# Kernel optimization log

Hardware: AMD Instinct MI355X
Metric: run time of the kernel (lower is better)

The kernel has to match this reference:

```python
import jax, jax.numpy as jnp
import numpy as np

HIDDEN = 256
HEADS = 8
HEAD_DIM = HIDDEN // HEADS
SCALE = HEAD_DIM ** -0.5


def setup_inputs() -> dict:
    key = jax.random.key(0)
    ks = jax.random.split(key, 12)
    B, N = 2, 2048
    s = lambda fan_in: 1.0 / np.sqrt(fan_in)
    inp = {
        'x': jax.random.normal(ks[0], (B, N, HIDDEN), jnp.float32),
        'coords': jax.random.normal(ks[1], (B, N, 3), jnp.float32),
        'W_qkv': jax.random.normal(ks[2], (HIDDEN, 3 * HIDDEN), jnp.float32) * s(HIDDEN),
        'W_out': jax.random.normal(ks[3], (HIDDEN, HIDDEN), jnp.float32) * s(HIDDEN),
        'b_out': jnp.zeros((HIDDEN,), jnp.float32),
        'pos_w1': jax.random.normal(ks[4], (3, 16), jnp.float32) * s(3),
        'pos_b1': jnp.zeros((16,), jnp.float32),
        'pos_w2': jax.random.normal(ks[5], (16, HEADS), jnp.float32) * s(16),
        'pos_b2': jnp.zeros((HEADS,), jnp.float32),
        'sym_w1': jax.random.normal(ks[6], (3, 16), jnp.float32) * s(3),
        'sym_b1': jnp.zeros((16,), jnp.float32),
        'sym_w2': jax.random.normal(ks[7], (16, HEADS), jnp.float32) * s(16),
        'sym_b2': jnp.zeros((HEADS,), jnp.float32),
    }
    return inp


def _bias_mlp(rel, w1, b1, w2, b2):
    # rel: [B,N,N,3] -> [B,H,N,N]
    h = jax.nn.relu(jnp.einsum('bijc,ck->bijk', rel, w1) + b1)
    out = jnp.einsum('bijk,kh->bijh', h, w2) + b2
    return jnp.transpose(out, (0, 3, 1, 2))


def reference(x, coords, W_qkv, W_out, b_out, pos_w1, pos_b1, pos_w2, pos_b2,
              sym_w1, sym_b1, sym_w2, sym_b2):
    B, N, C = x.shape
    qkv = (x @ W_qkv).reshape(B, N, 3, HEADS, HEAD_DIM)
    qkv = jnp.transpose(qkv, (2, 0, 3, 1, 4))  # [3,B,H,N,D]
    q, k, v = qkv[0], qkv[1], qkv[2]
    dots = jnp.einsum('bhid,bhjd->bhij', q, k) * SCALE
    rel_pos = coords[:, :, None, :] - coords[:, None, :, :]  # [B,N,N,3]
    reflect = jnp.array([-1.0, 1.0, 1.0], dtype=coords.dtype)
    coords_sym = coords * reflect
    sym_rel_pos = coords[:, :, None, :] - coords_sym[:, None, :, :]
    bias_direct = _bias_mlp(rel_pos, pos_w1, pos_b1, pos_w2, pos_b2)
    bias_sym = _bias_mlp(sym_rel_pos, sym_w1, sym_b1, sym_w2, sym_b2)
    attn = jax.nn.softmax(dots + bias_direct + bias_sym, axis=-1)
    out = jnp.einsum('bhij,bhjd->bhid', attn, v)
    out = jnp.transpose(out, (0, 2, 1, 3)).reshape(B, N, C)
    return out @ W_out + b_out
```

## Files before the change

kernel.cpp:

```cpp
#include <hip/hip_runtime.h>
#include <hip/hip_fp16.h>

typedef _Float16 half8_t __attribute__((ext_vector_type(8)));
typedef _Float16 half4_t __attribute__((ext_vector_type(4)));
typedef _Float16 h2      __attribute__((ext_vector_type(2)));
typedef float    f32x4   __attribute__((ext_vector_type(4)));

#define LOG2E 1.4426950408889634f
#define KSCALE (0.17677669529663687f * LOG2E)

#if __has_builtin(__builtin_amdgcn_exp2f)
#define EXP2F(x) __builtin_amdgcn_exp2f(x)
#else
#define EXP2F(x) exp2f(x)
#endif

template <int N>
__device__ __forceinline__ int dpp_ror(int v) {
  return __builtin_amdgcn_update_dpp(0, v, 0x120 + N, 0xf, 0xf, true);
}
__device__ __forceinline__ h2 rowmax16_h2(h2 v) {
  int t;
  t = dpp_ror<1>(__builtin_bit_cast(int, v));
  v = __builtin_elementwise_max(v, __builtin_bit_cast(h2, t));
  t = dpp_ror<2>(__builtin_bit_cast(int, v));
  v = __builtin_elementwise_max(v, __builtin_bit_cast(h2, t));
  t = dpp_ror<4>(__builtin_bit_cast(int, v));
  v = __builtin_elementwise_max(v, __builtin_bit_cast(h2, t));
  t = dpp_ror<8>(__builtin_bit_cast(int, v));
  v = __builtin_elementwise_max(v, __builtin_bit_cast(h2, t));
  return v;
}

__global__ __launch_bounds__(256) void prep_misc(
    const float* __restrict__ x, const float* __restrict__ Wqkv,
    const float* __restrict__ Wout, const float* __restrict__ coords,
    const float* __restrict__ pw1, const float* __restrict__ pb1,
    const float* __restrict__ sw1, const float* __restrict__ sb1,
    _Float16* __restrict__ xf16, _Float16* __restrict__ WqkvT,
    _Float16* __restrict__ WoutT, _Float16* __restrict__ APre,
    _Float16* __restrict__ BPre)
{
  __shared__ float tile[64][65];
  const int bi = blockIdx.x, tid = threadIdx.x;
  if (bi < 1024) {
    const int idx = bi * 256 + tid;
    f32x4 v = *reinterpret_cast<const f32x4*>(x + idx * 4);
    half4_t h;
    h[0] = (_Float16)v[0]; h[1] = (_Float16)v[1];
    h[2] = (_Float16)v[2]; h[3] = (_Float16)v[3];
    *reinterpret_cast<half4_t*>(xf16 + idx * 4) = h;
  } else if (bi < 1088) {
    const float* src; _Float16* dst; int t, W;
    if (bi < 1072) { t = bi - 1024; src = Wqkv; dst = WqkvT; W = 768; }
    else           { t = bi - 1072; src = Wout; dst = WoutT; W = 256; }
    const int nOT = W >> 6;
    const int tk = t / nOT, to = t % nOT;
    const int cx = tid & 63, ry = tid >> 6;
#pragma unroll
    for (int rr = 0; rr < 16; ++rr) {
      const int kl = rr * 4 + ry;
      tile[kl][cx] = src[(tk * 64 + kl) * W + to * 64 + cx];
    }
    __syncthreads();
#pragma unroll
    for (int rr = 0; rr < 16; ++rr) {
      const int ol = rr * 4 + ry;
      dst[(to * 64 + ol) * 256 + tk * 64 + cx] = (_Float16)tile[cx][ol];
    }
  } else {
    const int row = (bi - 1088) * 256 + tid;
    const float c0 = coords[row * 3 + 0];
    const float c1 = coords[row * 3 + 1];
    const float c2 = coords[row * 3 + 2];
#pragma unroll
    for (int k = 0; k < 16; ++k) {
      float a = c0 * pw1[k] + c1 * pw1[16 + k] + c2 * pw1[32 + k];
      APre[row * 32 + k] = (_Float16)(a + pb1[k]);
      BPre[row * 32 + k] = (_Float16)a;
      float s  =  c0 * sw1[k] + c1 * sw1[16 + k] + c2 * sw1[32 + k];
      float sb = -c0 * sw1[k] + c1 * sw1[16 + k] + c2 * sw1[32 + k];
      APre[row * 32 + 16 + k] = (_Float16)(s + sb1[k]);
      BPre[row * 32 + 16 + k] = (_Float16)sb;
    }
  }
}

__global__ __launch_bounds__(256) void qkv_gemm(
    const _Float16* __restrict__ xf16, const _Float16* __restrict__ WqkvT,
    _Float16* __restrict__ Qh, _Float16* __restrict__ Kh,
    _Float16* __restrict__ Vt)
{
  __shared__ _Float16 vtile[4][64][24];
  const int wv = threadIdx.x >> 6;
  const int wg = blockIdx.x * 4 + wv;
  const int ti = wg / 12, og = wg % 12;
  const int i0 = ti * 16, o0 = og * 64;
  const int lane = threadIdx.x & 63, q = lane >> 4, c = lane & 15;
  f32x4 acc[4] = {{0,0,0,0},{0,0,0,0},{0,0,0,0},{0,0,0,0}};
  const _Float16* arow = xf16 + (i0 + c) * 256;
  const _Float16* brow = WqkvT + (o0 + c) * 256;
#pragma unroll
  for (int k0 = 0; k0 < 256; k0 += 32) {
    half8_t af = *reinterpret_cast<const half8_t*>(arow + k0 + q * 8);
#pragma unroll
    for (int t = 0; t < 4; ++t) {
      half8_t bf = *reinterpret_cast<const half8_t*>(brow + t * 16 * 256 + k0 + q * 8);
      acc[t] = __builtin_amdgcn_mfma_f32_16x16x32_f16(af, bf, acc[t], 0, 0, 0);
    }
  }
  const int b = i0 >> 11, n0 = i0 & 2047;
  if (og < 8) {
#pragma unroll
    for (int t = 0; t < 4; ++t) {
      const int o = o0 + t * 16 + c;
      const int which = o >> 8, h = (o >> 5) & 7, d = o & 31;
#pragma unroll
      for (int r = 0; r < 4; ++r) {
        const int n = n0 + q * 4 + r;
        _Float16 v = (_Float16)acc[t][r];
        if (which == 0) Qh[((b * 8 + h) * 2048 + n) * 32 + d] = v;
        else            Kh[((b * 8 + h) * 2048 + n) * 32 + d] = v;
      }
    }
  } else {
    _Float16* vt = &vtile[wv][0][0];
#pragma unroll
    for (int t = 0; t < 4; ++t)
#pragma unroll
      for (int r = 0; r < 4; ++r)
        vt[(t * 16 + c) * 24 + q * 4 + r] = (_Float16)acc[t][r];
    asm volatile("s_waitcnt lgkmcnt(0)" ::: "memory");
    __builtin_amdgcn_sched_barrier(0);
    const long row = (long)(b * 256 + (o0 - 512) + lane);
    half8_t r0 = *reinterpret_cast<const half8_t*>(vt + lane * 24);
    half8_t r1 = *reinterpret_cast<const half8_t*>(vt + lane * 24 + 8);
    *reinterpret_cast<half8_t*>(Vt + row * 2048 + n0)     = r0;
    *reinterpret_cast<half8_t*>(Vt + row * 2048 + n0 + 8) = r1;
  }
}

__global__ __launch_bounds__(512, 4) void flash(
    const _Float16* __restrict__ Qh, const _Float16* __restrict__ Kh,
    const _Float16* __restrict__ Vt, const _Float16* __restrict__ APre,
    const _Float16* __restrict__ BPre, const float* __restrict__ pw2,
    const float* __restrict__ sw2, _Float16* __restrict__ Opart,
    float* __restrict__ Mpart)
{
  __shared__ __align__(16) unsigned char smem[53504];
  _Float16* biasH = reinterpret_cast<_Float16*>(smem);
  _Float16* pbuf  = reinterpret_cast<_Float16*>(smem + 37120);

  const int blk = blockIdx.x;
  const int b     = blk >> 8;
  const int chunk = (blk >> 6) & 3;
  const int i0    = (blk & 63) << 5;
  const int tid = threadIdx.x;
  const int w = tid >> 6, lane = tid & 63;
  const int q = lane >> 4, c = lane & 15;

  const _Float16* qbase = Qh + ((b * 8 + w) * 2048 + i0) * 32;
  half8_t qfA = *reinterpret_cast<const half8_t*>(qbase + c * 32 + q * 8);
  half8_t qfB = *reinterpret_cast<const half8_t*>(qbase + (16 + c) * 32 + q * 8);
  const _Float16* abase = APre + (b * 2048 + i0) * 32;
  half8_t apfA = *reinterpret_cast<const half8_t*>(abase + c * 32 + q * 8);
  half8_t apfB = *reinterpret_cast<const half8_t*>(abase + (16 + c) * 32 + q * 8);

  half8_t w2f;
#pragma unroll
  for (int jj = 0; jj < 8; ++jj) {
    const int k = q * 8 + jj;
    float val = 0.f;
    if (c < 8) val = (k < 16 ? pw2[k * 8 + c] : sw2[(k - 16) * 8 + c]) * LOG2E;
    w2f[jj] = (_Float16)val;
  }
  half8_t ones8;
#pragma unroll
  for (int jj = 0; jj < 8; ++jj) ones8[jj] = (_Float16)1.0f;

  float mA[4], mB[4];
  f32x4 O0A = {0,0,0,0}, O1A = {0,0,0,0}, O0B = {0,0,0,0}, O1B = {0,0,0,0};
  f32x4 lpA = {0,0,0,0}, lpB = {0,0,0,0};
#pragma unroll
  for (int r = 0; r < 4; ++r) { mA[r] = 0.f; mB[r] = 0.f; }

  const f32x4 z4 = {0.f, 0.f, 0.f, 0.f};
  half8_t hzero8 = {};

  const int jbase = chunk * 512;
  const _Float16* BPre_b = BPre + (long)b * 2048 * 32;
  _Float16* pbA = pbuf + w * 1024;
  _Float16* pbB = pbA + 512;

  for (int jt = 0; jt < 16; ++jt) {
    const int j0 = jbase + jt * 32;
    _Float16* bW = biasH + (jt & 1) * 9280;

#pragma unroll
    for (int mt = 0; mt < 4; ++mt) {
      const int jl = w * 4 + mt;
      half8_t bpf = *reinterpret_cast<const half8_t*>(
          BPre_b + (j0 + jl) * 32 + q * 8);
      half8_t hvA = __builtin_elementwise_max(apfA - bpf, hzero8);
      f32x4 bcA = __builtin_amdgcn_mfma_f32_16x16x32_f16(hvA, w2f, z4, 0, 0, 0);
      half8_t hvB = __builtin_elementwise_max(apfB - bpf, hzero8);
      f32x4 bcB = __builtin_amdgcn_mfma_f32_16x16x32_f16(hvB, w2f, z4, 0, 0, 0);
      if (c < 8) {
        half4_t b4;
        b4[0] = (_Float16)bcA[0]; b4[1] = (_Float16)bcA[1];
        b4[2] = (_Float16)bcA[2]; b4[3] = (_Float16)bcA[3];
        *reinterpret_cast<half4_t*>(bW + c * 1160 + jl * 36 + q * 4) = b4;
        half4_t b5;
        b5[0] = (_Float16)bcB[0]; b5[1] = (_Float16)bcB[1];
        b5[2] = (_Float16)bcB[2]; b5[3] = (_Float16)bcB[3];
        *reinterpret_cast<half4_t*>(bW + c * 1160 + jl * 36 + 16 + q * 4) = b5;
      }
    }

    const _Float16* kbase = Kh + ((b * 8 + w) * 2048 + j0) * 32;
    half8_t kf0 = *reinterpret_cast<const half8_t*>(kbase + (2 * c) * 32 + q * 8);
    half8_t kf1 = *reinterpret_cast<const half8_t*>(kbase + (2 * c + 1) * 32 + q * 8);
    const _Float16* vbase = Vt + (b * 8 + w) * 65536 + j0;
    half8_t vf0 = *reinterpret_cast<const half8_t*>(vbase + c * 2048 + q * 8);
    half8_t vf1 = *reinterpret_cast<const half8_t*>(vbase + (16 + c) * 2048 + q * 8);
    f32x4 sA0 = __builtin_amdgcn_mfma_f32_16x16x32_f16(qfA, kf0, z4, 0, 0, 0);
    f32x4 sA1 = __builtin_amdgcn_mfma_f32_16x16x32_f16(qfA, kf1, z4, 0, 0, 0);
    f32x4 sB0 = __builtin_amdgcn_mfma_f32_16x16x32_f16(qfB, kf0, z4, 0, 0, 0);
    f32x4 sB1 = __builtin_amdgcn_mfma_f32_16x16x32_f16(qfB, kf1, z4, 0, 0, 0);

    __syncthreads();

    const _Float16* bR = biasH + (jt & 1) * 9280 + w * 1160;
    half4_t bbA0 = *reinterpret_cast<const half4_t*>(bR + (2 * c) * 36 + q * 4);
    half4_t bbA1 = *reinterpret_cast<const half4_t*>(bR + (2 * c + 1) * 36 + q * 4);
    half4_t bbB0 = *reinterpret_cast<const half4_t*>(bR + (2 * c) * 36 + 16 + q * 4);
    half4_t bbB1 = *reinterpret_cast<const half4_t*>(bR + (2 * c + 1) * 36 + 16 + q * 4);

    {
      float sv0[4], sv1[4], p0[4], p1[4], mr[4];
#pragma unroll
      for (int r = 0; r < 4; ++r) {
        sv0[r] = sA0[r] * KSCALE + (float)bbA0[r];
        sv1[r] = sA1[r] * KSCALE + (float)bbA1[r];
        mr[r] = fmaxf(sv0[r], sv1[r]);
      }
#pragma unroll
      for (int r = 0; r < 4; ++r) {
        p0[r] = EXP2F(sv0[r] - mA[r]);
        p1[r] = EXP2F(sv1[r] - mA[r]);
      }
      float need = fmaxf(fmaxf(mr[0] - mA[0], mr[1] - mA[1]),
                         fmaxf(mr[2] - mA[2], mr[3] - mA[3]));
      if (__any(need > 4.0f)) {
        h2 pk01, pk23;
        pk01[0] = (_Float16)mr[0]; pk01[1] = (_Float16)mr[1];
        pk23[0] = (_Float16)mr[2]; pk23[1] = (_Float16)mr[3];
        pk01 = rowmax16_h2(pk01);
        pk23 = rowmax16_h2(pk23);
        float mred[4] = {(float)pk01[0], (float)pk01[1],
                         (float)pk23[0], (float)pk23[1]};
#pragma unroll
        for (int r = 0; r < 4; ++r) {
          const float mnew = fmaxf(mA[r], mred[r]);
          const float alpha = EXP2F(mA[r] - mnew);
          p0[r] *= alpha; p1[r] *= alpha;
          lpA[r] *= alpha;
          O0A[r] *= alpha; O1A[r] *= alpha;
          mA[r] = mnew;
        }
      }
#pragma unroll
      for (int r = 0; r < 4; ++r) {
        h2 pp; pp[0] = (_Float16)p0[r]; pp[1] = (_Float16)p1[r];
        *reinterpret_cast<h2*>(pbA + (q * 4 + r) * 32 + 2 * c) = pp;
      }
    }
    {
      float sv0[4], sv1[4], p0[4], p1[4], mr[4];
#pragma unroll
      for (int r = 0; r < 4; ++r) {
        sv0[r] = sB0[r] * KSCALE + (float)bbB0[r];
        sv1[r] = sB1[r] * KSCALE + (float)bbB1[r];
        mr[r] = fmaxf(sv0[r], sv1[r]);
      }
#pragma unroll
      for (int r = 0; r < 4; ++r) {
        p0[r] = EXP2F(sv0[r] - mB[r]);
        p1[r] = EXP2F(sv1[r] - mB[r]);
      }
      float need = fmaxf(fmaxf(mr[0] - mB[0], mr[1] - mB[1]),
                         fmaxf(mr[2] - mB[2], mr[3] - mB[3]));
      if (__any(need > 4.0f)) {
        h2 pk01, pk23;
        pk01[0] = (_Float16)mr[0]; pk01[1] = (_Float16)mr[1];
        pk23[0] = (_Float16)mr[2]; pk23[1] = (_Float16)mr[3];
        pk01 = rowmax16_h2(pk01);
        pk23 = rowmax16_h2(pk23);
        float mred[4] = {(float)pk01[0], (float)pk01[1],
                         (float)pk23[0], (float)pk23[1]};
#pragma unroll
        for (int r = 0; r < 4; ++r) {
          const float mnew = fmaxf(mB[r], mred[r]);
          const float alpha = EXP2F(mB[r] - mnew);
          p0[r] *= alpha; p1[r] *= alpha;
          lpB[r] *= alpha;
          O0B[r] *= alpha; O1B[r] *= alpha;
          mB[r] = mnew;
        }
      }
#pragma unroll
      for (int r = 0; r < 4; ++r) {
        h2 pp; pp[0] = (_Float16)p0[r]; pp[1] = (_Float16)p1[r];
        *reinterpret_cast<h2*>(pbB + (q * 4 + r) * 32 + 2 * c) = pp;
      }
    }

    asm volatile("s_waitcnt lgkmcnt(0)" ::: "memory");
    __builtin_amdgcn_sched_barrier(0);

    half8_t pfA = *reinterpret_cast<const half8_t*>(pbA + c * 32 + q * 8);
    half8_t pfB = *reinterpret_cast<const half8_t*>(pbB + c * 32 + q * 8);
    O0A = __builtin_amdgcn_mfma_f32_16x16x32_f16(pfA, vf0, O0A, 0, 0, 0);
    O1A = __builtin_amdgcn_mfma_f32_16x16x32_f16(pfA, vf1, O1A, 0, 0, 0);
    O0B = __builtin_amdgcn_mfma_f32_16x16x32_f16(pfB, vf0, O0B, 0, 0, 0);
    O1B = __builtin_amdgcn_mfma_f32_16x16x32_f16(pfB, vf1, O1B, 0, 0, 0);
    lpA = __builtin_amdgcn_mfma_f32_16x16x32_f16(pfA, ones8, lpA, 0, 0, 0);
    lpB = __builtin_amdgcn_mfma_f32_16x16x32_f16(pfB, ones8, lpB, 0, 0, 0);
  }

#pragma unroll
  for (int r = 0; r < 4; ++r) {
    const float s = lpA[r];
    const float inv = 1.f / s;
    const int n = i0 + q * 4 + r;
    const long base = (long)(((chunk * 2 + b) * 8 + w) * 2048 + n);
    Opart[base * 32 + c]      = (_Float16)(O0A[r] * inv);
    Opart[base * 32 + 16 + c] = (_Float16)(O1A[r] * inv);
    if (c == 0) Mpart[base] = mA[r] + __log2f(s);
  }
#pragma unroll
  for (int r = 0; r < 4; ++r) {
    const float s = lpB[r];
    const float inv = 1.f / s;
    const int n = i0 + 16 + q * 4 + r;
    const long base = (long)(((chunk * 2 + b) * 8 + w) * 2048 + n);
    Opart[base * 32 + c]      = (_Float16)(O0B[r] * inv);
    Opart[base * 32 + 16 + c] = (_Float16)(O1B[r] * inv);
    if (c == 0) Mpart[base] = mB[r] + __log2f(s);
  }
}

__global__ __launch_bounds__(256) void combine_proj(
    const _Float16* __restrict__ Opart, const float* __restrict__ Mpart,
    const _Float16* __restrict__ WoutT, const float* __restrict__ bout,
    float* __restrict__ out)
{
  __shared__ _Float16 aT[16][264];
  const int i0 = blockIdx.x * 16;
  const int b = i0 >> 11;
  const int n0 = i0 & 2047;
  const int tid = threadIdx.x;
  {
    const int row = tid >> 4, cg = tid & 15;
    const int n = n0 + row;
    const int h = cg >> 1;
    const int d0 = (cg & 1) * 16;
    float mv[4], M = -INFINITY;
#pragma unroll
    for (int ck = 0; ck < 4; ++ck) {
      mv[ck] = Mpart[((ck * 2 + b) * 8 + h) * 2048 + n];
      M = fmaxf(M, mv[ck]);
    }
    float num[16];
#pragma unroll
    for (int e = 0; e < 16; ++e) num[e] = 0.f;
    float den = 0.f;
#pragma unroll
    for (int ck = 0; ck < 4; ++ck) {
      const float wgt = EXP2F(mv[ck] - M);
      const _Float16* op = Opart +
          (long)(((ck * 2 + b) * 8 + h) * 2048 + n) * 32 + d0;
      half8_t o0v = *reinterpret_cast<const half8_t*>(op);
      half8_t o1v = *reinterpret_cast<const half8_t*>(op + 8);
#pragma unroll
      for (int e = 0; e < 8; ++e) {
        num[e]     += wgt * (float)o0v[e];
        num[8 + e] += wgt * (float)o1v[e];
      }
      den += wgt;
    }
    const float inv = 1.f / den;
    half8_t h0, h1;
#pragma unroll
    for (int e = 0; e < 8; ++e) {
      h0[e] = (_Float16)(num[e] * inv);
      h1[e] = (_Float16)(num[8 + e] * inv);
    }
    *reinterpret_cast<half8_t*>(&aT[row][cg * 16])     = h0;
    *reinterpret_cast<half8_t*>(&aT[row][cg * 16 + 8]) = h1;
  }
  __syncthreads();

  const int o0 = (tid >> 6) * 64;
  const int lane = tid & 63, q = lane >> 4, c = lane & 15;
  f32x4 acc[4] = {{0,0,0,0},{0,0,0,0},{0,0,0,0},{0,0,0,0}};
  const _Float16* brow = WoutT + (o0 + c) * 256;
#pragma unroll
  for (int k0 = 0; k0 < 256; k0 += 32) {
    half8_t af = *reinterpret_cast<const half8_t*>(&aT[c][k0 + q * 8]);
#pragma unroll
    for (int t = 0; t < 4; ++t) {
      half8_t bf = *reinterpret_cast<const half8_t*>(brow + t * 16 * 256 + k0 + q * 8);
      acc[t] = __builtin_amdgcn_mfma_f32_16x16x32_f16(af, bf, acc[t], 0, 0, 0);
    }
  }
#pragma unroll
  for (int t = 0; t < 4; ++t) {
    const float bo = bout[o0 + t * 16 + c];
#pragma unroll
    for (int r = 0; r < 4; ++r)
      out[(i0 + q * 4 + r) * 256 + o0 + t * 16 + c] = acc[t][r] + bo;
  }
}

extern "C" void kernel_launch(void* const* d_in, const int* in_sizes, int n_in,
                              void* d_out, int out_size, void* d_ws, size_t ws_size,
                              hipStream_t stream)
{
  const float* x      = (const float*)d_in[0];
  const float* coords = (const float*)d_in[1];
  const float* Wqkv   = (const float*)d_in[2];
  const float* Wout   = (const float*)d_in[3];
  const float* bout   = (const float*)d_in[4];
  const float* pw1    = (const float*)d_in[5];
  const float* pb1    = (const float*)d_in[6];
  const float* pw2    = (const float*)d_in[7];
  const float* sw1    = (const float*)d_in[9];
  const float* sb1    = (const float*)d_in[10];
  const float* sw2    = (const float*)d_in[11];
  float* out = (float*)d_out;

  char* ws = (char*)d_ws;
  _Float16* Qh      = (_Float16*)(ws + 0);
  _Float16* Kh      = (_Float16*)(ws + 2097152);
  _Float16* Vt      = (_Float16*)(ws + 4194304);
  _Float16* xf16    = (_Float16*)(ws + 6291456);
  _Float16* WqkvT   = (_Float16*)(ws + 8388608);
  _Float16* WoutT   = (_Float16*)(ws + 8781824);
  _Float16* APre    = (_Float16*)(ws + 8912896);
  _Float16* BPre    = (_Float16*)(ws + 9175040);
  _Float16* Opart   = (_Float16*)(ws + 9437184);
  float*    Mpart   = (float*)   (ws + 17825792);

  prep_misc<<<1104, 256, 0, stream>>>(x, Wqkv, Wout, coords, pw1, pb1, sw1, sb1,
                                      xf16, WqkvT, WoutT, APre, BPre);
  qkv_gemm<<<768, 256, 0, stream>>>(xf16, WqkvT, Qh, Kh, Vt);
  flash<<<512, 512, 0, stream>>>(Qh, Kh, Vt, APre, BPre, pw2, sw2, Opart, Mpart);
  combine_proj<<<256, 256, 0, stream>>>(Opart, Mpart, WoutT, bout, out);
}
```

Measured before the change: 170.4 us.

## Fuse x fp32-to-fp16 conversion into QKV GEMM and stage Q/K stores via LDS

The separate pass that converted x to fp16 in prep_misc is removed. qkv_gemm now loads x as fp32 and converts it in registers before the MFMA, which drops a full write and reread of the fp16 copy of x. The Q/K epilogue now transposes the accumulators through LDS so it can issue 16-byte vector stores instead of scattered 2-byte stores. In exchange the GEMM reads twice as many bytes for its A operand, and each x row is reloaded and reconverted by all 12 output-group waves.

```diff
diff --git a/kernel.cpp b/kernel.cpp
--- a/kernel.cpp
+++ b/kernel.cpp
@@ -33,27 +33,19 @@
 }
 
 __global__ __launch_bounds__(256) void prep_misc(
-    const float* __restrict__ x, const float* __restrict__ Wqkv,
-    const float* __restrict__ Wout, const float* __restrict__ coords,
+    const float* __restrict__ Wqkv, const float* __restrict__ Wout,
+    const float* __restrict__ coords,
     const float* __restrict__ pw1, const float* __restrict__ pb1,
     const float* __restrict__ sw1, const float* __restrict__ sb1,
-    _Float16* __restrict__ xf16, _Float16* __restrict__ WqkvT,
-    _Float16* __restrict__ WoutT, _Float16* __restrict__ APre,
-    _Float16* __restrict__ BPre)
+    _Float16* __restrict__ WqkvT, _Float16* __restrict__ WoutT,
+    _Float16* __restrict__ APre, _Float16* __restrict__ BPre)
 {
   __shared__ float tile[64][65];
   const int bi = blockIdx.x, tid = threadIdx.x;
-  if (bi < 1024) {
-    const int idx = bi * 256 + tid;
-    f32x4 v = *reinterpret_cast<const f32x4*>(x + idx * 4);
-    half4_t h;
-    h[0] = (_Float16)v[0]; h[1] = (_Float16)v[1];
-    h[2] = (_Float16)v[2]; h[3] = (_Float16)v[3];
-    *reinterpret_cast<half4_t*>(xf16 + idx * 4) = h;
-  } else if (bi < 1088) {
+  if (bi < 64) {
     const float* src; _Float16* dst; int t, W;
-    if (bi < 1072) { t = bi - 1024; src = Wqkv; dst = WqkvT; W = 768; }
-    else           { t = bi - 1072; src = Wout; dst = WoutT; W = 256; }
+    if (bi < 48) { t = bi;      src = Wqkv; dst = WqkvT; W = 768; }
+    else         { t = bi - 48; src = Wout; dst = WoutT; W = 256; }
     const int nOT = W >> 6;
     const int tk = t / nOT, to = t % nOT;
     const int cx = tid & 63, ry = tid >> 6;
@@ -69,7 +61,7 @@
       dst[(to * 64 + ol) * 256 + tk * 64 + cx] = (_Float16)tile[cx][ol];
     }
   } else {
-    const int row = (bi - 1088) * 256 + tid;
+    const int row = (bi - 64) * 256 + tid;
     const float c0 = coords[row * 3 + 0];
     const float c1 = coords[row * 3 + 1];
     const float c2 = coords[row * 3 + 2];
@@ -87,22 +79,28 @@
 }
 
 __global__ __launch_bounds__(256) void qkv_gemm(
-    const _Float16* __restrict__ xf16, const _Float16* __restrict__ WqkvT,
+    const float* __restrict__ x, const _Float16* __restrict__ WqkvT,
     _Float16* __restrict__ Qh, _Float16* __restrict__ Kh,
     _Float16* __restrict__ Vt)
 {
-  __shared__ _Float16 vtile[4][64][24];
+  __shared__ __align__(16) _Float16 tbuf[4][1536];
   const int wv = threadIdx.x >> 6;
   const int wg = blockIdx.x * 4 + wv;
   const int ti = wg / 12, og = wg % 12;
   const int i0 = ti * 16, o0 = og * 64;
   const int lane = threadIdx.x & 63, q = lane >> 4, c = lane & 15;
   f32x4 acc[4] = {{0,0,0,0},{0,0,0,0},{0,0,0,0},{0,0,0,0}};
-  const _Float16* arow = xf16 + (i0 + c) * 256;
+  const float*    arow = x + (i0 + c) * 256;
   const _Float16* brow = WqkvT + (o0 + c) * 256;
 #pragma unroll
   for (int k0 = 0; k0 < 256; k0 += 32) {
-    half8_t af = *reinterpret_cast<const half8_t*>(arow + k0 + q * 8);
+    f32x4 a0 = *reinterpret_cast<const f32x4*>(arow + k0 + q * 8);
+    f32x4 a1 = *reinterpret_cast<const f32x4*>(arow + k0 + q * 8 + 4);
+    half8_t af;
+    af[0] = (_Float16)a0[0]; af[1] = (_Float16)a0[1];
+    af[2] = (_Float16)a0[2]; af[3] = (_Float16)a0[3];
+    af[4] = (_Float16)a1[0]; af[5] = (_Float16)a1[1];
+    af[6] = (_Float16)a1[2]; af[7] = (_Float16)a1[3];
 #pragma unroll
     for (int t = 0; t < 4; ++t) {
       half8_t bf = *reinterpret_cast<const half8_t*>(brow + t * 16 * 256 + k0 + q * 8);
@@ -110,21 +108,25 @@
     }
   }
   const int b = i0 >> 11, n0 = i0 & 2047;
+  _Float16* vt = tbuf[wv];
   if (og < 8) {
 #pragma unroll
-    for (int t = 0; t < 4; ++t) {
-      const int o = o0 + t * 16 + c;
-      const int which = o >> 8, h = (o >> 5) & 7, d = o & 31;
-#pragma unroll
-      for (int r = 0; r < 4; ++r) {
-        const int n = n0 + q * 4 + r;
-        _Float16 v = (_Float16)acc[t][r];
-        if (which == 0) Qh[((b * 8 + h) * 2048 + n) * 32 + d] = v;
-        else            Kh[((b * 8 + h) * 2048 + n) * 32 + d] = v;
-      }
-    }
+    for (int t = 0; t < 4; ++t)
+#pragma unroll
+      for (int r = 0; r < 4; ++r)
+        vt[(q * 4 + r) * 72 + t * 16 + c] = (_Float16)acc[t][r];
+    asm volatile("s_waitcnt lgkmcnt(0)" ::: "memory");
+    __builtin_amdgcn_sched_barrier(0);
+    const int nl = lane & 15, seg = lane >> 4;
+    const int o_g = o0 + seg * 16;
+    const int h = (o_g >> 5) & 7, dbase = o_g & 31;
+    _Float16* dst = ((o_g >> 8) == 0 ? Qh : Kh) +
+                    ((b * 8 + h) * 2048 + n0 + nl) * 32 + dbase;
+    half8_t r0 = *reinterpret_cast<const half8_t*>(vt + nl * 72 + seg * 16);
+    half8_t r1 = *reinterpret_cast<const half8_t*>(vt + nl * 72 + seg * 16 + 8);
+    *reinterpret_cast<half8_t*>(dst)     = r0;
+    *reinterpret_cast<half8_t*>(dst + 8) = r1;
   } else {
-    _Float16* vt = &vtile[wv][0][0];
 #pragma unroll
     for (int t = 0; t < 4; ++t)
 #pragma unroll
@@ -444,7 +446,6 @@
   _Float16* Qh      = (_Float16*)(ws + 0);
   _Float16* Kh      = (_Float16*)(ws + 2097152);
   _Float16* Vt      = (_Float16*)(ws + 4194304);
-  _Float16* xf16    = (_Float16*)(ws + 6291456);
   _Float16* WqkvT   = (_Float16*)(ws + 8388608);
   _Float16* WoutT   = (_Float16*)(ws + 8781824);
   _Float16* APre    = (_Float16*)(ws + 8912896);
@@ -452,9 +453,9 @@
   _Float16* Opart   = (_Float16*)(ws + 9437184);
   float*    Mpart   = (float*)   (ws + 17825792);
 
-  prep_misc<<<1104, 256, 0, stream>>>(x, Wqkv, Wout, coords, pw1, pb1, sw1, sb1,
-                                      xf16, WqkvT, WoutT, APre, BPre);
-  qkv_gemm<<<768, 256, 0, stream>>>(xf16, WqkvT, Qh, Kh, Vt);
+  prep_misc<<<80, 256, 0, stream>>>(Wqkv, Wout, coords, pw1, pb1, sw1, sb1,
+                                    WqkvT, WoutT, APre, BPre);
+  qkv_gemm<<<768, 256, 0, stream>>>(x, WqkvT, Qh, Kh, Vt);
   flash<<<512, 512, 0, stream>>>(Qh, Kh, Vt, APre, BPre, pw2, sw2, Opart, Mpart);
   combine_proj<<<256, 256, 0, stream>>>(Opart, Mpart, WoutT, bout, out);
 }
```

Result: no change. 170.9 us (+0.3%).
